# Kernel optimization log

Measured on AMD Instinct MI355X. Metric: run time of the kernel, lower is better.

Reference implementation:

```python
import jax, jax.numpy as jnp
import numpy as np

B = 64
H = W = 16
DIMS = [2048, 1024, 512, 256, 128, 1]


def setup_inputs() -> dict:
    key = jax.random.key(0)
    ks = jax.random.split(key, 11)
    inp = {"x": jax.random.normal(ks[0], (B, DIMS[0], H, W), dtype=jnp.float32)}
    for i in range(5):
        fan_in = DIMS[i]
        out = DIMS[i + 1]
        # per-sample weights [B, out, in, 1, 1], scaled ~1/sqrt(fan_in) to keep sigmoids unsaturated
        inp[f"fc{i+1}w"] = jax.random.normal(ks[1 + 2 * i], (B, out, fan_in, 1, 1), dtype=jnp.float32) / jnp.sqrt(jnp.float32(fan_in))
        inp[f"fc{i+1}b"] = jax.random.normal(ks[2 + 2 * i], (B, out), dtype=jnp.float32) * 0.1
    return inp


def _target_fc(h, w, b):
    # grouped 1x1 conv with groups=B == per-sample linear over channel dim
    # h: [B, in, H, W], w: [B, out, in, 1, 1], b: [B, out] -> [B, out, H, W]
    return jnp.einsum("boi,bihw->bohw", w[..., 0, 0], h) + b[:, :, None, None]


def reference(x, fc1w, fc1b, fc2w, fc2b, fc3w, fc3b, fc4w, fc4b, fc5w, fc5b):
    q = jax.nn.sigmoid(_target_fc(x, fc1w, fc1b))
    q = jax.nn.sigmoid(_target_fc(q, fc2w, fc2b))
    q = jax.nn.sigmoid(_target_fc(q, fc3w, fc3b))
    q = jax.nn.sigmoid(_target_fc(q, fc4w, fc4b))
    q = _target_fc(q, fc5w, fc5b)  # [B, 1, H, W]
    q = jnp.squeeze(q, axis=1)      # .squeeze() -> [B, H, W]
    return jax.nn.sigmoid(q)
```

## Files before the change

kernel.cpp:

```cpp
#include <hip/hip_runtime.h>
#include <hip/hip_bf16.h>
#include <hip/hip_fp16.h>


typedef __attribute__((ext_vector_type(4)))  float    f32x4;
typedef __attribute__((ext_vector_type(16))) float    f32x16;
typedef __attribute__((ext_vector_type(8)))  short    short8;
typedef __attribute__((ext_vector_type(4)))  short    short4v;
typedef __attribute__((ext_vector_type(8)))  _Float16 half8;

__device__ __forceinline__ unsigned short f2h_bits(float f) {
  return __builtin_bit_cast(unsigned short, (_Float16)f);
}
__device__ __forceinline__ float h2f(short h) {
  return (float)__builtin_bit_cast(_Float16, (unsigned short)h);
}

__global__ __launch_bounds__(256) void transpose_cvt(const float* __restrict__ X,
                                                     short* __restrict__ XT) {
  __shared__ float tile[32][33];
  const int b  = blockIdx.z;
  const int c0 = blockIdx.x * 32, s0 = blockIdx.y * 32;
  const int tl = threadIdx.x & 31, tw = threadIdx.x >> 5;
  const float* xp = X + ((size_t)b * 2048 + c0) * 256 + s0;
#pragma unroll
  for (int i = 0; i < 4; ++i) {
    const int c = tw * 4 + i;
    tile[c][tl] = xp[(size_t)c * 256 + tl];
  }
  __syncthreads();
  short* op = XT + ((size_t)(b * 256 + s0)) * 2048 + c0;
#pragma unroll
  for (int i = 0; i < 4; ++i) {
    const int s = tw * 4 + i;
    op[(size_t)s * 2048 + tl] = (short)f2h_bits(tile[tl][s]);
  }
}

template <int BK> struct WFrag { f32x4 v[BK / 8]; };

template <int M, int K, int WAVES, int NSPLIT, int BK, bool FUSE5>
__global__ __launch_bounds__(WAVES * 64, 2) void gemm_layer(
    const float* __restrict__ W, const float* __restrict__ bias,
    const short* __restrict__ Xin, short* __restrict__ Out,
    const float* __restrict__ W5, const float* __restrict__ B5,
    float* __restrict__ out5) {
  constexpr int KH    = BK / 16;
  constexpr int NT    = K / BK;
  constexpr int NCG   = 8 / NSPLIT;
  constexpr int TILES = NCG * KH;
  constexpr int BM    = WAVES * 32;
  constexpr int MT    = M / BM;
  constexpr int TPW   = TILES / WAVES;
  constexpr int NS    = 256 / NSPLIT;
  constexpr int EPIW  = 40;
  constexpr int PERB  = MT * NSPLIT;

  __shared__ __align__(16) short lds[2][TILES * 512];
  __shared__ __align__(16) short epi[WAVES][32][EPIW];

  const int tid = threadIdx.x;
  const int w = tid >> 6, l = tid & 63;
  const int lr = l & 31;
  const int lh = l >> 5;

  const int bid = blockIdx.x;
  const int xcd = bid & 7;
  const int i_  = bid >> 3;
  const int b   = xcd + 8 * (i_ / PERB);
  const int rem = i_ % PERB;
  const int mt  = rem / NSPLIT;
  const int ns  = rem % NSPLIT;
  const int m0  = mt * BM + w * 32;

  const float* Wb = W + ((size_t)b * M + m0) * K;
  const short* Xb = Xin + (size_t)b * 256 * K + (size_t)ns * NS * K;

  f32x16 acc[NCG] = {};

  auto stage = [&](int buf, int t) {
    const int k0 = t * BK;
#pragma unroll
    for (int i = 0; i < TPW; ++i) {
      const int T  = w * TPW + i;
      const int s  = (T / KH) * 32 + lr;
      const int kk = (T % KH) * 16 + (lh << 3);
      const short* src = Xb + (size_t)s * K + k0 + kk;
      __builtin_amdgcn_global_load_lds(
          (const __attribute__((address_space(1))) void*)src,
          (__attribute__((address_space(3))) void*)&lds[buf][T * 512],
          16, 0, 0);
    }
  };

  const float* wrow = Wb + (size_t)lr * K + (lh << 3);
  auto load_wfrag = [&](int t) {
    WFrag<BK> f;
#pragma unroll
    for (int h = 0; h < KH; ++h) {
      const float* wp = wrow + t * BK + h * 16;
      f.v[2 * h]     = *(const f32x4*)wp;
      f.v[2 * h + 1] = *(const f32x4*)(wp + 4);
    }
    return f;
  };

  WFrag<BK> wn;
  half8 wcH[KH];
  auto cvtW = [&]() {
#pragma unroll
    for (int h = 0; h < KH; ++h) {
#pragma unroll
      for (int j = 0; j < 4; ++j) {
        wcH[h][j]     = (_Float16)wn.v[2 * h][j];
        wcH[h][j + 4] = (_Float16)wn.v[2 * h + 1][j];
      }
    }
  };

  stage(0, 0);
  asm volatile("" ::: "memory");
  wn = load_wfrag(0);
  asm volatile("" ::: "memory");
  stage(1, 1);
  asm volatile("" ::: "memory");
  cvtW();
  wn = load_wfrag(1);
  asm volatile("" ::: "memory");
  asm volatile("s_barrier" ::: "memory");
  __builtin_amdgcn_sched_barrier(0);

  for (int t = 0; t < NT; ++t) {
    const int cur = t & 1;
#pragma unroll
    for (int h = 0; h < KH; ++h) {
#pragma unroll
      for (int cg = 0; cg < NCG; ++cg) {
        const short8 braw = *(const short8*)&lds[cur][(cg * KH + h) * 512 + l * 8];
        acc[cg] = __builtin_amdgcn_mfma_f32_32x32x16_f16(wcH[h], __builtin_bit_cast(half8, braw),
                                                         acc[cg], 0, 0, 0);
      }
    }
    if (t + 1 < NT) {
      if constexpr (BK == 128) {
        asm volatile("s_waitcnt vmcnt(16)" ::: "memory");
      } else {
        asm volatile("s_waitcnt vmcnt(8)" ::: "memory");
      }
      __builtin_amdgcn_sched_barrier(0);
      asm volatile("s_barrier" ::: "memory");
      __builtin_amdgcn_sched_barrier(0);
      if (t + 2 < NT) {
        stage(cur, t + 2);
        asm volatile("" ::: "memory");
      }
      cvtW();
      if (t + 2 < NT) {
        wn = load_wfrag(t + 2);
        asm volatile("" ::: "memory");
      }
    }
  }

  float brow[16];
#pragma unroll
  for (int r = 0; r < 16; ++r) {
    const int row = (r & 3) + 8 * (r >> 2) + (lh << 2);
    brow[r] = bias[(size_t)b * M + m0 + row];
  }
  const int s_loc = l >> 1, hi = l & 1;
#pragma unroll
  for (int cg = 0; cg < NCG; ++cg) {
#pragma unroll
    for (int rg = 0; rg < 4; ++rg) {
      short4v pk;
#pragma unroll
      for (int j = 0; j < 4; ++j) {
        const int r = rg * 4 + j;
        float v = acc[cg][r] + brow[r];
        v = 1.0f / (1.0f + __expf(-v));
        pk[j] = (short)f2h_bits(v);
      }
      *(short4v*)&epi[w][lr][rg * 8 + (lh << 2)] = pk;
    }
    if constexpr (!FUSE5) {
      const short8 r0 = *(const short8*)&epi[w][s_loc][hi * 16];
      const short8 r1 = *(const short8*)&epi[w][s_loc][hi * 16 + 8];
      short* op = Out + ((size_t)b * 256 + ns * NS + cg * 32 + s_loc) * M + m0 + hi * 16;
      *(short8*)op       = r0;
      *(short8*)(op + 8) = r1;
    } else {
      static_assert(!FUSE5 || (M == 128 && WAVES == 4), "FUSE5 needs full-M 4-wave block");
      __syncthreads();
      const int s_ = tid >> 3, r_ = tid & 7;
      const short8 h0 = *(const short8*)&epi[r_ >> 1][s_][(r_ & 1) * 16];
      const short8 h1 = *(const short8*)&epi[r_ >> 1][s_][(r_ & 1) * 16 + 8];
      const float* wp = W5 + b * 128 + r_ * 16;
      const f32x4 w0 = *(const f32x4*)wp;
      const f32x4 w1 = *(const f32x4*)(wp + 4);
      const f32x4 w2 = *(const f32x4*)(wp + 8);
      const f32x4 w3 = *(const f32x4*)(wp + 12);
      float a = 0.f;
#pragma unroll
      for (int j = 0; j < 4; ++j) a += h2f(h0[j]) * w0[j];
#pragma unroll
      for (int j = 0; j < 4; ++j) a += h2f(h0[j + 4]) * w1[j];
#pragma unroll
      for (int j = 0; j < 4; ++j) a += h2f(h1[j]) * w2[j];
#pragma unroll
      for (int j = 0; j < 4; ++j) a += h2f(h1[j + 4]) * w3[j];
      a += __shfl_xor(a, 1);
      a += __shfl_xor(a, 2);
      a += __shfl_xor(a, 4);
      if (r_ == 0) out5[b * 256 + ns * NS + cg * 32 + s_] = 1.0f / (1.0f + __expf(-(a + B5[b])));
      __syncthreads();
    }
  }
}

extern "C" void kernel_launch(void* const* d_in, const int* in_sizes, int n_in,
                              void* d_out, int out_size, void* d_ws, size_t ws_size,
                              hipStream_t stream) {
  const float* x  = (const float*)d_in[0];
  const float* w1 = (const float*)d_in[1];  const float* b1 = (const float*)d_in[2];
  const float* w2 = (const float*)d_in[3];  const float* b2 = (const float*)d_in[4];
  const float* w3 = (const float*)d_in[5];  const float* b3 = (const float*)d_in[6];
  const float* w4 = (const float*)d_in[7];  const float* b4 = (const float*)d_in[8];
  const float* w5 = (const float*)d_in[9];  const float* b5 = (const float*)d_in[10];

  char* ws = (char*)d_ws;
  short* bufA = (short*)ws;
  short* bufB = (short*)(ws + (size_t)67108864);
  float* out  = (float*)d_out;

  transpose_cvt<<<dim3(64, 8, 64), 256, 0, stream>>>(x, bufA);
  gemm_layer<1024, 2048, 8, 1, 64, false><<<256, 512, 0, stream>>>(
      w1, b1, bufA, bufB, nullptr, nullptr, nullptr);
  gemm_layer<512, 1024, 4, 1, 64, false><<<256, 256, 0, stream>>>(
      w2, b2, bufB, bufA, nullptr, nullptr, nullptr);
  gemm_layer<256, 512, 4, 2, 64, false><<<256, 256, 0, stream>>>(
      w3, b3, bufA, bufB, nullptr, nullptr, nullptr);
  gemm_layer<128, 256, 4, 4, 64, true><<<256, 256, 0, stream>>>(
      w4, b4, bufB, nullptr, w5, b5, out);
}
```

Baseline: 304.9 us.

## Fuse layers 2-5 into one kernel with per-sample global barriers

Layers 2 through 5 now run as phases of a single persistent kernel instead of three separate launches. Within each sample, the four blocks synchronise through an atomic-counter barrier in global memory, and the counters are zeroed by the transpose kernel. This saves two launch boundaries and the drain/ramp gaps between them. In exchange it depends on all 256 blocks being co-resident, since the spin barrier could deadlock otherwise, and it adds atomic polling overhead.

```diff
diff --git a/kernel.cpp b/kernel.cpp
--- a/kernel.cpp
+++ b/kernel.cpp
@@ -17,7 +17,10 @@
 }
 
 __global__ __launch_bounds__(256) void transpose_cvt(const float* __restrict__ X,
-                                                     short* __restrict__ XT) {
+                                                     short* __restrict__ XT,
+                                                     int* __restrict__ flags) {
+  if (blockIdx.x == 0 && blockIdx.y == 0 && blockIdx.z == 0 && threadIdx.x < 64)
+    flags[threadIdx.x] = 0;
   __shared__ float tile[32][33];
   const int b  = blockIdx.z;
   const int c0 = blockIdx.x * 32, s0 = blockIdx.y * 32;
@@ -40,11 +43,12 @@
 template <int BK> struct WFrag { f32x4 v[BK / 8]; };
 
 template <int M, int K, int WAVES, int NSPLIT, int BK, bool FUSE5>
-__global__ __launch_bounds__(WAVES * 64, 2) void gemm_layer(
+__device__ __forceinline__ void gemm_phase(
+    short* __restrict__ ldsb, short* __restrict__ epi,
     const float* __restrict__ W, const float* __restrict__ bias,
     const short* __restrict__ Xin, short* __restrict__ Out,
     const float* __restrict__ W5, const float* __restrict__ B5,
-    float* __restrict__ out5) {
+    float* __restrict__ out5, const int b, const int rem, const int tid) {
   constexpr int KH    = BK / 16;
   constexpr int NT    = K / BK;
   constexpr int NCG   = 8 / NSPLIT;
@@ -54,24 +58,13 @@
   constexpr int TPW   = TILES / WAVES;
   constexpr int NS    = 256 / NSPLIT;
   constexpr int EPIW  = 40;
-  constexpr int PERB  = MT * NSPLIT;
-
-  __shared__ __align__(16) short lds[2][TILES * 512];
-  __shared__ __align__(16) short epi[WAVES][32][EPIW];
-
-  const int tid = threadIdx.x;
+  constexpr int LHALF = TILES * 512;
+  (void)MT;
+
   const int w = tid >> 6, l = tid & 63;
-  const int lr = l & 31;
-  const int lh = l >> 5;
-
-  const int bid = blockIdx.x;
-  const int xcd = bid & 7;
-  const int i_  = bid >> 3;
-  const int b   = xcd + 8 * (i_ / PERB);
-  const int rem = i_ % PERB;
-  const int mt  = rem / NSPLIT;
-  const int ns  = rem % NSPLIT;
-  const int m0  = mt * BM + w * 32;
+  const int lr = l & 31, lh = l >> 5;
+  const int mt = rem / NSPLIT, ns = rem % NSPLIT;
+  const int m0 = mt * BM + w * 32;
 
   const float* Wb = W + ((size_t)b * M + m0) * K;
   const short* Xb = Xin + (size_t)b * 256 * K + (size_t)ns * NS * K;
@@ -88,7 +81,7 @@
       const short* src = Xb + (size_t)s * K + k0 + kk;
       __builtin_amdgcn_global_load_lds(
           (const __attribute__((address_space(1))) void*)src,
-          (__attribute__((address_space(3))) void*)&lds[buf][T * 512],
+          (__attribute__((address_space(3))) void*)&ldsb[buf * LHALF + T * 512],
           16, 0, 0);
     }
   };
@@ -136,7 +129,7 @@
     for (int h = 0; h < KH; ++h) {
 #pragma unroll
       for (int cg = 0; cg < NCG; ++cg) {
-        const short8 braw = *(const short8*)&lds[cur][(cg * KH + h) * 512 + l * 8];
+        const short8 braw = *(const short8*)&ldsb[cur * LHALF + (cg * KH + h) * 512 + l * 8];
         acc[cg] = __builtin_amdgcn_mfma_f32_32x32x16_f16(wcH[h], __builtin_bit_cast(half8, braw),
                                                          acc[cg], 0, 0, 0);
       }
@@ -168,6 +161,7 @@
     const int row = (r & 3) + 8 * (r >> 2) + (lh << 2);
     brow[r] = bias[(size_t)b * M + m0 + row];
   }
+  auto ep = [&](int wi, int s, int i) { return &epi[(((wi << 5) + s) * EPIW) + i]; };
   const int s_loc = l >> 1, hi = l & 1;
 #pragma unroll
   for (int cg = 0; cg < NCG; ++cg) {
@@ -181,11 +175,11 @@
         v = 1.0f / (1.0f + __expf(-v));
         pk[j] = (short)f2h_bits(v);
       }
-      *(short4v*)&epi[w][lr][rg * 8 + (lh << 2)] = pk;
+      *(short4v*)ep(w, lr, rg * 8 + (lh << 2)) = pk;
     }
     if constexpr (!FUSE5) {
-      const short8 r0 = *(const short8*)&epi[w][s_loc][hi * 16];
-      const short8 r1 = *(const short8*)&epi[w][s_loc][hi * 16 + 8];
+      const short8 r0 = *(const short8*)ep(w, s_loc, hi * 16);
+      const short8 r1 = *(const short8*)ep(w, s_loc, hi * 16 + 8);
       short* op = Out + ((size_t)b * 256 + ns * NS + cg * 32 + s_loc) * M + m0 + hi * 16;
       *(short8*)op       = r0;
       *(short8*)(op + 8) = r1;
@@ -193,8 +187,8 @@
       static_assert(!FUSE5 || (M == 128 && WAVES == 4), "FUSE5 needs full-M 4-wave block");
       __syncthreads();
       const int s_ = tid >> 3, r_ = tid & 7;
-      const short8 h0 = *(const short8*)&epi[r_ >> 1][s_][(r_ & 1) * 16];
-      const short8 h1 = *(const short8*)&epi[r_ >> 1][s_][(r_ & 1) * 16 + 8];
+      const short8 h0 = *(const short8*)ep(r_ >> 1, s_, (r_ & 1) * 16);
+      const short8 h1 = *(const short8*)ep(r_ >> 1, s_, (r_ & 1) * 16 + 8);
       const float* wp = W5 + b * 128 + r_ * 16;
       const f32x4 w0 = *(const f32x4*)wp;
       const f32x4 w1 = *(const f32x4*)(wp + 4);
@@ -216,6 +210,56 @@
       __syncthreads();
     }
   }
+}
+
+template <int M, int K, int WAVES, int NSPLIT, int BK>
+__global__ __launch_bounds__(WAVES * 64, 2) void gemm_layer(
+    const float* __restrict__ W, const float* __restrict__ bias,
+    const short* __restrict__ Xin, short* __restrict__ Out) {
+  constexpr int NCG = 8 / NSPLIT, KH = BK / 16, TILES = NCG * KH;
+  constexpr int PERB = (M / (WAVES * 32)) * NSPLIT;
+  __shared__ __align__(16) short ldsb[2 * TILES * 512];
+  __shared__ __align__(16) short epi[WAVES * 32 * 40];
+  const int tid = threadIdx.x, bid = blockIdx.x;
+  const int xcd = bid & 7, i_ = bid >> 3;
+  const int b = xcd + 8 * (i_ / PERB);
+  const int rem = i_ % PERB;
+  gemm_phase<M, K, WAVES, NSPLIT, BK, false>(ldsb, epi, W, bias, Xin, Out,
+                                             nullptr, nullptr, nullptr, b, rem, tid);
+}
+
+__device__ __forceinline__ void sample_barrier(int* flag, int target, int tid) {
+  __syncthreads();
+  if (tid == 0) {
+    __threadfence();
+    atomicAdd(flag, 1);
+    while (atomicAdd(flag, 0) < target) __builtin_amdgcn_s_sleep(2);
+    __threadfence();
+  }
+  __syncthreads();
+}
+
+__global__ __launch_bounds__(256, 2) void tail_fused(
+    const float* __restrict__ W2, const float* __restrict__ b2,
+    const float* __restrict__ W3, const float* __restrict__ b3,
+    const float* __restrict__ W4, const float* __restrict__ b4,
+    const float* __restrict__ W5, const float* __restrict__ B5,
+    const short* __restrict__ h1, short* __restrict__ h2, short* __restrict__ h3,
+    float* __restrict__ out, int* __restrict__ flags) {
+  __shared__ __align__(16) short ldsb[2 * 32 * 512];
+  __shared__ __align__(16) short epi[4 * 32 * 40];
+  const int tid = threadIdx.x, bid = blockIdx.x;
+  const int xcd = bid & 7, i_ = bid >> 3;
+  const int b = xcd + 8 * (i_ >> 2);
+  const int rem = i_ & 3;
+  gemm_phase<512, 1024, 4, 1, 64, false>(ldsb, epi, W2, b2, h1, h2,
+                                         nullptr, nullptr, nullptr, b, rem, tid);
+  sample_barrier(&flags[b], 4, tid);
+  gemm_phase<256, 512, 4, 2, 64, false>(ldsb, epi, W3, b3, h2, h3,
+                                        nullptr, nullptr, nullptr, b, rem, tid);
+  sample_barrier(&flags[b], 8, tid);
+  gemm_phase<128, 256, 4, 4, 64, true>(ldsb, epi, W4, b4, h3, nullptr,
+                                       W5, B5, out, b, rem, tid);
 }
 
 extern "C" void kernel_launch(void* const* d_in, const int* in_sizes, int n_in,
@@ -229,17 +273,15 @@
   const float* w5 = (const float*)d_in[9];  const float* b5 = (const float*)d_in[10];
 
   char* ws = (char*)d_ws;
-  short* bufA = (short*)ws;
-  short* bufB = (short*)(ws + (size_t)67108864);
-  float* out  = (float*)d_out;
-
-  transpose_cvt<<<dim3(64, 8, 64), 256, 0, stream>>>(x, bufA);
-  gemm_layer<1024, 2048, 8, 1, 64, false><<<256, 512, 0, stream>>>(
-      w1, b1, bufA, bufB, nullptr, nullptr, nullptr);
-  gemm_layer<512, 1024, 4, 1, 64, false><<<256, 256, 0, stream>>>(
-      w2, b2, bufB, bufA, nullptr, nullptr, nullptr);
-  gemm_layer<256, 512, 4, 2, 64, false><<<256, 256, 0, stream>>>(
-      w3, b3, bufA, bufB, nullptr, nullptr, nullptr);
-  gemm_layer<128, 256, 4, 4, 64, true><<<256, 256, 0, stream>>>(
-      w4, b4, bufB, nullptr, w5, b5, out);
-}
+  short* xT    = (short*)ws;
+  short* h1    = (short*)(ws + 67108864ull);
+  short* h2    = (short*)(ws + 102760448ull);
+  short* h3    = (short*)(ws + 120586240ull);
+  int*   flags = (int*)  (ws + 130023424ull);
+  float* out   = (float*)d_out;
+
+  transpose_cvt<<<dim3(64, 8, 64), 256, 0, stream>>>(x, xT, flags);
+  gemm_layer<1024, 2048, 8, 1, 64><<<256, 512, 0, stream>>>(w1, b1, xT, h1);
+  tail_fused<<<256, 256, 0, stream>>>(w2, b2, w3, b3, w4, b4, w5, b5,
+                                      h1, h2, h3, out, flags);
+}
```

Result: slower. 345.7 us (+13.4%).
